# Performance work log

Measured on AMD Instinct MI355X. Metric: run time of the kernel, lower is better.

## Reference

```python
import jax, jax.numpy as jnp
import numpy as np

NX, NY, C, B, P = 432, 496, 64, 4, 40000


def setup_inputs() -> dict:
    key = jax.random.key(0)
    k1, _ = jax.random.split(key)
    pillar_features = jax.random.normal(k1, (P, C), dtype=jnp.float32)
    # Build voxel_coords with unique (x, y) cells per batch element so the
    # scatter-write has no duplicate indices (matches deterministic torch assignment).
    rng = np.random.default_rng(0)
    per = P // B  # pillars per sample
    coords = np.empty((P, 3), dtype=np.int64)
    for b in range(B):
        flat = rng.choice(NX * NY, size=per, replace=False)
        coords[b * per:(b + 1) * per, 0] = flat % NX          # x index
        coords[b * per:(b + 1) * per, 1] = flat // NX         # y index
        coords[b * per:(b + 1) * per, 2] = b                  # batch index (last col)
    return {
        "pillar_features": pillar_features,
        "voxel_coords": jnp.asarray(coords),
        "batch_size": B,
        "nx": NX,
        "ny": NY,
    }


def reference(pillar_features, voxel_coords, batch_size, nx, ny):
    # Fused scatter: compute a global flat index (batch, y, x) for every pillar
    # and scatter all pillars in a single pass (no per-batch masking loop).
    x = voxel_coords[:, 0]
    y = voxel_coords[:, 1]
    b = voxel_coords[:, -1]
    flat = b * (ny * nx) + y * nx + x                       # [P]
    c = pillar_features.shape[1]
    grid = jnp.zeros((batch_size * ny * nx, c), dtype=pillar_features.dtype)
    grid = grid.at[flat].set(pillar_features)               # scatter pillars
    # [B*ny*nx, C] -> [B, C, ny, nx]
    return grid.reshape(batch_size, ny, nx, c).transpose(0, 3, 1, 2)
```

## Files before the change

### kernel.cpp

```cpp
#include <hip/hip_runtime.h>


__global__ void scatter_kernel(const float* __restrict__ feat,
                               const int* __restrict__ coords,
                               int n_pillars, int C,
                               const int* __restrict__ nx_p,
                               const int* __restrict__ ny_p,
                               float* __restrict__ out) {
    const long long t = (long long)blockIdx.x * blockDim.x + threadIdx.x;
    if (t >= (long long)n_pillars * C) return;

    int p, c;
    if (C == 64) {
        p = (int)(t >> 6);
        c = (int)(t & 63);
    } else {
        p = (int)(t / C);
        c = (int)(t - (long long)p * C);
    }

    const int nx = nx_p[0];
    const int ny = ny_p[0];
    const int plane = nx * ny;

    const int x = coords[3 * p + 0];
    const int y = coords[3 * p + 1];
    const int b = coords[3 * p + 2];

    const float v = feat[t];

    const size_t o = ((size_t)b * C + c) * (size_t)plane + (size_t)y * nx + x;
    out[o] = v;
}

extern "C" void kernel_launch(void* const* d_in, const int* in_sizes, int n_in,
                              void* d_out, int out_size, void* d_ws, size_t ws_size,
                              hipStream_t stream) {
    const float* feat   = (const float*)d_in[0];
    const int*   coords = (const int*)d_in[1];
    const int* nx_p = (const int*)d_in[3];
    const int* ny_p = (const int*)d_in[4];
    float* out = (float*)d_out;

    const int n_pillars = in_sizes[1] / 3;
    const int C = in_sizes[0] / n_pillars;

    (void)hipMemsetAsync(out, 0, (size_t)out_size * sizeof(float), stream);

    const long long total = (long long)n_pillars * C;
    const unsigned nblocks = (unsigned)((total + 255) / 256);
    scatter_kernel<<<nblocks, 256, 0, stream>>>(
        feat, coords, n_pillars, C, nx_p, ny_p, out);
}
```

Measured before the change: 252.5 us.

## Replace memset+scatter with inverse slot map and single coalesced write sweep

Builds an inverse map from grid cell to pillar index (16-bit slots) and a channel-major transposed copy of the features. A single persistent kernel then sweeps the whole output once with vectorized float4 stores, gathering features where slots are occupied and writing zeros elsewhere. This removes the separate full-output memset and the uncoalesced scattered writes, at the cost of extra small kernels, workspace use and gather reads. The original scatter path is kept as a fallback when shape assumptions fail.

```diff
diff --git a/kernel.cpp b/kernel.cpp
--- a/kernel.cpp
+++ b/kernel.cpp
@@ -1,36 +1,105 @@
 #include <hip/hip_runtime.h>
 
 
-__global__ void scatter_kernel(const float* __restrict__ feat,
-                               const int* __restrict__ coords,
-                               int n_pillars, int C,
-                               const int* __restrict__ nx_p,
-                               const int* __restrict__ ny_p,
-                               float* __restrict__ out) {
-    const long long t = (long long)blockIdx.x * blockDim.x + threadIdx.x;
-    if (t >= (long long)n_pillars * C) return;
+#define C_CH 64
+#define WNB  512
+#define WBT  256
 
-    int p, c;
-    if (C == 64) {
-        p = (int)(t >> 6);
-        c = (int)(t & 63);
-    } else {
-        p = (int)(t / C);
-        c = (int)(t - (long long)p * C);
-    }
+typedef float fvec4 __attribute__((ext_vector_type(4)));
 
+__global__ void build_slots_kernel(const int* __restrict__ coords, int n_pillars,
+                                   const int* __restrict__ nx_p,
+                                   const int* __restrict__ ny_p,
+                                   unsigned short* __restrict__ slot_of) {
+    int p = blockIdx.x * blockDim.x + threadIdx.x;
+    if (p >= n_pillars) return;
     const int nx = nx_p[0];
     const int ny = ny_p[0];
-    const int plane = nx * ny;
-
     const int x = coords[3 * p + 0];
     const int y = coords[3 * p + 1];
     const int b = coords[3 * p + 2];
+    const long long m = (long long)b * (long long)(nx * ny) + (long long)y * nx + x;
+    slot_of[m] = (unsigned short)p;
+}
 
-    const float v = feat[t];
+__global__ void transpose_feat_kernel(const float* __restrict__ feat,
+                                      float* __restrict__ featT,
+                                      int n_pillars, int Ppad) {
+    const int t = blockIdx.x * blockDim.x + threadIdx.x;
+    if (t >= n_pillars * C_CH) return;
+    const int p = t >> 6;
+    const int c = t & 63;
+    featT[(size_t)c * Ppad + p] = feat[t];
+}
 
+__global__ __launch_bounds__(WBT) void write_sweep_kernel(
+    const float* __restrict__ featT, const unsigned short* __restrict__ slot_of,
+    const int* __restrict__ nx_p, const int* __restrict__ ny_p,
+    float* __restrict__ out, int total_quads, int Ppad, int nb) {
+    const int plane = nx_p[0] * ny_p[0];
+    const int plane_q = plane >> 2;
+    const int t = threadIdx.x;
+    const int w = t >> 6;
+    const int l = t & 63;
+
+    for (int Qb = blockIdx.x * 4096; Qb < total_quads; Qb += nb * 4096) {
+        int Q = Qb + w * 1024 + l;
+        int bc = (int)((unsigned)Q / (unsigned)plane_q);
+        int q  = Q - bc * plane_q;
+        int c  = bc & 63;
+        int b  = bc >> 6;
+        int ci = b * plane + 4 * q;
+        const float* frow = featT + (size_t)c * Ppad;
+
+#pragma unroll
+        for (int j = 0; j < 16; ++j) {
+            const int Qj = Q + 64 * j;
+            if (Qj < total_quads) {
+                const unsigned long long sl =
+                    *reinterpret_cast<const unsigned long long*>(slot_of + ci);
+                fvec4 v = (fvec4)0.0f;
+                if (sl != ~0ull) {
+                    const unsigned s0 = (unsigned)sl & 0xFFFFu;
+                    const unsigned s1 = (unsigned)(sl >> 16) & 0xFFFFu;
+                    const unsigned s2 = (unsigned)(sl >> 32) & 0xFFFFu;
+                    const unsigned s3 = (unsigned)(sl >> 48);
+                    if (s0 != 0xFFFFu) v.x = frow[s0];
+                    if (s1 != 0xFFFFu) v.y = frow[s1];
+                    if (s2 != 0xFFFFu) v.z = frow[s2];
+                    if (s3 != 0xFFFFu) v.w = frow[s3];
+                }
+                reinterpret_cast<fvec4*>(out)[Qj] = v;
+            }
+            q += 64;
+            ci += 256;
+            if (q >= plane_q) {
+                q -= plane_q;
+                if (c == 63) { c = 0; ++b; }
+                else         { ++c; ci -= plane; }
+                frow = featT + (size_t)c * Ppad;
+            }
+        }
+    }
+}
+
+__global__ void direct_scatter_kernel(const float* __restrict__ feat,
+                                      const int* __restrict__ coords,
+                                      int n_pillars, int C,
+                                      const int* __restrict__ nx_p,
+                                      const int* __restrict__ ny_p,
+                                      float* __restrict__ out) {
+    const long long t = (long long)blockIdx.x * blockDim.x + threadIdx.x;
+    if (t >= (long long)n_pillars * C) return;
+    const int p = (int)(t / C);
+    const int c = (int)(t - (long long)p * C);
+    const int nx = nx_p[0];
+    const int ny = ny_p[0];
+    const int x = coords[3 * p + 0];
+    const int y = coords[3 * p + 1];
+    const int b = coords[3 * p + 2];
+    const int plane = nx * ny;
     const size_t o = ((size_t)b * C + c) * (size_t)plane + (size_t)y * nx + x;
-    out[o] = v;
+    out[o] = feat[(size_t)p * C + c];
 }
 
 extern "C" void kernel_launch(void* const* d_in, const int* in_sizes, int n_in,
@@ -44,11 +113,32 @@
 
     const int n_pillars = in_sizes[1] / 3;
     const int C = in_sizes[0] / n_pillars;
+    const int n_map = out_size / C;
+    const int Ppad = (n_pillars + 63) & ~63;
 
-    (void)hipMemsetAsync(out, 0, (size_t)out_size * sizeof(float), stream);
+    const size_t slot_bytes  = (size_t)n_map * sizeof(unsigned short);
+    const size_t featT_off   = (slot_bytes + 255) & ~(size_t)255;
+    const size_t featT_bytes = (size_t)C_CH * Ppad * sizeof(float);
+    const size_t need = featT_off + featT_bytes;
 
-    const long long total = (long long)n_pillars * C;
-    const unsigned nblocks = (unsigned)((total + 255) / 256);
-    scatter_kernel<<<nblocks, 256, 0, stream>>>(
-        feat, coords, n_pillars, C, nx_p, ny_p, out);
+    if (C == C_CH && n_pillars < 65535 && ws_size >= need &&
+        (out_size % (C_CH * 4)) == 0) {
+        unsigned short* slot_of = (unsigned short*)d_ws;
+        float* featT = (float*)((char*)d_ws + featT_off);
+
+        (void)hipMemsetAsync(slot_of, 0xFF, slot_bytes, stream);
+        build_slots_kernel<<<(n_pillars + 255) / 256, 256, 0, stream>>>(
+            coords, n_pillars, nx_p, ny_p, slot_of);
+        transpose_feat_kernel<<<(n_pillars * C_CH + 255) / 256, 256, 0, stream>>>(
+            feat, featT, n_pillars, Ppad);
+
+        const int total_quads = (out_size / 4);
+        write_sweep_kernel<<<WNB, WBT, 0, stream>>>(
+            featT, slot_of, nx_p, ny_p, out, total_quads, Ppad, WNB);
+    } else {
+        (void)hipMemsetAsync(out, 0, (size_t)out_size * sizeof(float), stream);
+        const long long total = (long long)n_pillars * C;
+        direct_scatter_kernel<<<(unsigned)((total + 255) / 256), 256, 0, stream>>>(
+            feat, coords, n_pillars, C, nx_p, ny_p, out);
+    }
 }
```

New measurement: 318.1 us. +26.0%, slower.
